# Kernel optimization log

Hardware: AMD Instinct MI355X
Metric: run time of the kernel (lower is better)

The kernel has to match this reference:

```python
import jax, jax.numpy as jnp
import numpy as np

FEATURES_NUM = 125388  # shogi halfKP: 81 king squares * 1548
L1, L2, L3 = 256, 32, 32
BATCH = 1024
ACTIVE = 38  # typical number of active halfKP features per position


def _sparse_multi_hot(key, batch, nfeat, active):
    idx = jax.random.randint(key, (batch, active), 0, nfeat)
    rows = jnp.arange(batch)[:, None]
    x = jnp.zeros((batch, nfeat), dtype=jnp.float32)
    return x.at[rows, idx].set(1.0)


def setup_inputs() -> dict:
    key = jax.random.key(0)
    ks = jax.random.split(key, 10)
    s_in = 1.0 / np.sqrt(FEATURES_NUM)
    s1 = 1.0 / np.sqrt(2 * L1)
    s2 = 1.0 / np.sqrt(L2)
    s3 = 1.0 / np.sqrt(L3)
    return {
        "x1": _sparse_multi_hot(ks[0], BATCH, FEATURES_NUM, ACTIVE),
        "x2": _sparse_multi_hot(ks[1], BATCH, FEATURES_NUM, ACTIVE),
        "W_in": jax.random.normal(ks[2], (FEATURES_NUM, L1), jnp.float32) * s_in,
        "b_in": jax.random.normal(ks[3], (L1,), jnp.float32) * s_in,
        "W1": jax.random.normal(ks[4], (2 * L1, L2), jnp.float32) * s1,
        "b1": jax.random.normal(ks[5], (L2,), jnp.float32) * s1,
        "W2": jax.random.normal(ks[6], (L2, L3), jnp.float32) * s2,
        "b2": jax.random.normal(ks[7], (L3,), jnp.float32) * s2,
        "Wo": jax.random.normal(ks[8], (L3, 1), jnp.float32) * s3,
        "bo": jax.random.normal(ks[9], (1,), jnp.float32) * s3,
    }


def reference(x1, x2, W_in, b_in, W1, b1, W2, b2, Wo, bo):
    # Feature transformer: shared input_layer on both perspectives.
    a1 = x1 @ W_in + b_in              # [B, L1]
    a2 = x2 @ W_in + b_in              # [B, L1]
    x = jnp.concatenate([a1, a2], axis=1)      # [B, 2*L1]
    x = jnp.clip(x, 0.0, 1.0)                   # clipped ReLU
    x = jnp.clip(x @ W1 + b1, 0.0, 1.0)         # [B, L2]
    x = jnp.clip(x @ W2 + b2, 0.0, 1.0)         # [B, L3]
    return x @ Wo + bo                          # [B, 1]
```

## Files before the change

### kernel.cpp

```cpp
#include <hip/hip_runtime.h>

#define FEAT  125388
#define VEC4  (FEAT / 4)
#define L1    256
#define L2    32
#define L3    32
#define BATCH 1024
#define CAP   64

typedef unsigned int uint4_ev __attribute__((ext_vector_type(4)));

__global__ __launch_bounds__(256) void nnue_scan_ft(
    const float* __restrict__ x1, const float* __restrict__ x2,
    const float* __restrict__ W_in, const float* __restrict__ b_in,
    float* __restrict__ x_cat)
{
    const int bp = blockIdx.x;
    const int b  = bp >> 1;
    const int p  = bp & 1;
    const int t  = threadIdx.x;

    __shared__ int s_idx[CAP];
    __shared__ int s_cnt;
    if (t == 0) s_cnt = 0;
    __syncthreads();

    const float* base = (p == 0 ? x1 : x2) + (size_t)b * FEAT;
    const uint4_ev* row = reinterpret_cast<const uint4_ev*>(base);

    for (int iv = t; iv < VEC4; iv += 256) {
        uint4_ev v = __builtin_nontemporal_load(&row[iv]);
        if (v.x | v.y | v.z | v.w) {
            #pragma unroll
            for (int c = 0; c < 4; ++c) {
                if (v[c] != 0u) {
                    int slot = atomicAdd(&s_cnt, 1);
                    if (slot < CAP) s_idx[slot] = iv * 4 + c;
                }
            }
        }
    }
    __syncthreads();

    const int n = min(s_cnt, CAP);
    float acc = b_in[t];
    for (int i = 0; i < n; ++i)
        acc += W_in[(size_t)s_idx[i] * L1 + t];

    x_cat[(size_t)b * (2 * L1) + p * L1 + t] = fminf(fmaxf(acc, 0.f), 1.f);
}

__global__ __launch_bounds__(256) void nnue_tail(
    const float* __restrict__ x_cat,
    const float* __restrict__ W1, const float* __restrict__ b1,
    const float* __restrict__ W2, const float* __restrict__ b2,
    const float* __restrict__ Wo, const float* __restrict__ bo,
    float* __restrict__ out)
{
    const int b = blockIdx.x;
    const int t = threadIdx.x;

    __shared__ float s_x[2 * L1];
    __shared__ float s_part[8][L2];
    __shared__ float s_y[L2];
    __shared__ float s_o[L3];

    s_x[t]       = x_cat[(size_t)b * (2 * L1) + t];
    s_x[t + 256] = x_cat[(size_t)b * (2 * L1) + 256 + t];
    __syncthreads();

    {
        const int j  = t & 31;
        const int p  = t >> 5;
        const int k0 = p * 64;
        float acc = 0.f;
        #pragma unroll 4
        for (int k = k0; k < k0 + 64; ++k)
            acc += s_x[k] * W1[k * L2 + j];
        s_part[p][j] = acc;
    }
    __syncthreads();
    if (t < L2) {
        float acc = b1[t];
        #pragma unroll
        for (int p = 0; p < 8; ++p) acc += s_part[p][t];
        s_y[t] = fminf(fmaxf(acc, 0.f), 1.f);
    }
    __syncthreads();
    if (t < L3) {
        float acc = b2[t];
        #pragma unroll
        for (int k = 0; k < L2; ++k) acc += s_y[k] * W2[k * L3 + t];
        s_o[t] = fminf(fmaxf(acc, 0.f), 1.f) * Wo[t];
    }
    __syncthreads();
    if (t == 0) {
        float acc = bo[0];
        #pragma unroll
        for (int k = 0; k < L3; ++k) acc += s_o[k];
        out[b] = acc;
    }
}

extern "C" void kernel_launch(void* const* d_in, const int* in_sizes, int n_in,
                              void* d_out, int out_size, void* d_ws, size_t ws_size,
                              hipStream_t stream) {
    const float* x1   = (const float*)d_in[0];
    const float* x2   = (const float*)d_in[1];
    const float* W_in = (const float*)d_in[2];
    const float* b_in = (const float*)d_in[3];
    const float* W1   = (const float*)d_in[4];
    const float* b1   = (const float*)d_in[5];
    const float* W2   = (const float*)d_in[6];
    const float* b2   = (const float*)d_in[7];
    const float* Wo   = (const float*)d_in[8];
    const float* bo   = (const float*)d_in[9];
    float* out   = (float*)d_out;
    float* x_cat = (float*)d_ws;

    nnue_scan_ft<<<2 * BATCH, 256, 0, stream>>>(x1, x2, W_in, b_in, x_cat);
    nnue_tail<<<BATCH, 256, 0, stream>>>(x_cat, W1, b1, W2, b2, Wo, bo, out);
}
```

Baseline: 179.8 us.

## Fuse scan/feature-transform and MLP tail via last-block atomic counter

Merges the two kernels into one. Each batch row's two perspective blocks increment a per-row atomic flag, and the second block to finish runs the small MLP tail using its own accumulator plus the partner's result from global memory. This removes the separate tail launch and one global reload, at the cost of a memset launch per call, threadfences, and extra shared memory per block.

Result: slower. 510.9 us (+184.2%).

```diff
diff --git a/kernel.cpp b/kernel.cpp
--- a/kernel.cpp
+++ b/kernel.cpp
@@ -10,24 +10,34 @@
 
 typedef unsigned int uint4_ev __attribute__((ext_vector_type(4)));
 
-__global__ __launch_bounds__(256) void nnue_scan_ft(
+__global__ __launch_bounds__(256) void nnue_fused(
     const float* __restrict__ x1, const float* __restrict__ x2,
     const float* __restrict__ W_in, const float* __restrict__ b_in,
-    float* __restrict__ x_cat)
+    const float* __restrict__ W1, const float* __restrict__ b1,
+    const float* __restrict__ W2, const float* __restrict__ b2,
+    const float* __restrict__ Wo, const float* __restrict__ bo,
+    float* __restrict__ x_cat,
+    int*   __restrict__ flags,
+    float* __restrict__ out)
 {
     const int bp = blockIdx.x;
     const int b  = bp >> 1;
     const int p  = bp & 1;
     const int t  = threadIdx.x;
 
-    __shared__ int s_idx[CAP];
-    __shared__ int s_cnt;
+    __shared__ int   s_idx[CAP];
+    __shared__ int   s_cnt;
+    __shared__ int   s_last;
+    __shared__ float s_x[2 * L1];
+    __shared__ float s_part[8][L2];
+    __shared__ float s_y[L2];
+    __shared__ float s_o[L3];
+
     if (t == 0) s_cnt = 0;
     __syncthreads();
 
     const float* base = (p == 0 ? x1 : x2) + (size_t)b * FEAT;
     const uint4_ev* row = reinterpret_cast<const uint4_ev*>(base);
-
     for (int iv = t; iv < VEC4; iv += 256) {
         uint4_ev v = __builtin_nontemporal_load(&row[iv]);
         if (v.x | v.y | v.z | v.w) {
@@ -46,59 +56,54 @@
     float acc = b_in[t];
     for (int i = 0; i < n; ++i)
         acc += W_in[(size_t)s_idx[i] * L1 + t];
+    const float v_own = fminf(fmaxf(acc, 0.f), 1.f);
 
-    x_cat[(size_t)b * (2 * L1) + p * L1 + t] = fminf(fmaxf(acc, 0.f), 1.f);
-}
+    x_cat[(size_t)b * (2 * L1) + p * L1 + t] = v_own;
+    __threadfence();
+    __syncthreads();
+    if (t == 0) {
+        int old = __hip_atomic_fetch_add(&flags[b], 1, __ATOMIC_ACQ_REL,
+                                         __HIP_MEMORY_SCOPE_AGENT);
+        s_last = old;
+    }
+    __syncthreads();
+    if (s_last != 1) return;
+    __threadfence();
 
-__global__ __launch_bounds__(256) void nnue_tail(
-    const float* __restrict__ x_cat,
-    const float* __restrict__ W1, const float* __restrict__ b1,
-    const float* __restrict__ W2, const float* __restrict__ b2,
-    const float* __restrict__ Wo, const float* __restrict__ bo,
-    float* __restrict__ out)
-{
-    const int b = blockIdx.x;
-    const int t = threadIdx.x;
-
-    __shared__ float s_x[2 * L1];
-    __shared__ float s_part[8][L2];
-    __shared__ float s_y[L2];
-    __shared__ float s_o[L3];
-
-    s_x[t]       = x_cat[(size_t)b * (2 * L1) + t];
-    s_x[t + 256] = x_cat[(size_t)b * (2 * L1) + 256 + t];
+    s_x[p * L1 + t]       = v_own;
+    s_x[(1 - p) * L1 + t] = x_cat[(size_t)b * (2 * L1) + (1 - p) * L1 + t];
     __syncthreads();
 
     {
         const int j  = t & 31;
-        const int p  = t >> 5;
-        const int k0 = p * 64;
-        float acc = 0.f;
+        const int pc = t >> 5;
+        const int k0 = pc * 64;
+        float a1 = 0.f;
         #pragma unroll 4
         for (int k = k0; k < k0 + 64; ++k)
-            acc += s_x[k] * W1[k * L2 + j];
-        s_part[p][j] = acc;
+            a1 += s_x[k] * W1[k * L2 + j];
+        s_part[pc][j] = a1;
     }
     __syncthreads();
     if (t < L2) {
-        float acc = b1[t];
+        float a1 = b1[t];
         #pragma unroll
-        for (int p = 0; p < 8; ++p) acc += s_part[p][t];
-        s_y[t] = fminf(fmaxf(acc, 0.f), 1.f);
+        for (int pc = 0; pc < 8; ++pc) a1 += s_part[pc][t];
+        s_y[t] = fminf(fmaxf(a1, 0.f), 1.f);
     }
     __syncthreads();
     if (t < L3) {
-        float acc = b2[t];
+        float a2 = b2[t];
         #pragma unroll
-        for (int k = 0; k < L2; ++k) acc += s_y[k] * W2[k * L3 + t];
-        s_o[t] = fminf(fmaxf(acc, 0.f), 1.f) * Wo[t];
+        for (int k = 0; k < L2; ++k) a2 += s_y[k] * W2[k * L3 + t];
+        s_o[t] = fminf(fmaxf(a2, 0.f), 1.f) * Wo[t];
     }
     __syncthreads();
     if (t == 0) {
-        float acc = bo[0];
+        float a3 = bo[0];
         #pragma unroll
-        for (int k = 0; k < L3; ++k) acc += s_o[k];
-        out[b] = acc;
+        for (int k = 0; k < L3; ++k) a3 += s_o[k];
+        out[b] = a3;
     }
 }
 
@@ -116,8 +121,11 @@
     const float* Wo   = (const float*)d_in[8];
     const float* bo   = (const float*)d_in[9];
     float* out   = (float*)d_out;
+
     float* x_cat = (float*)d_ws;
+    int*   flags = (int*)((char*)d_ws + (size_t)BATCH * 2 * L1 * sizeof(float));
 
-    nnue_scan_ft<<<2 * BATCH, 256, 0, stream>>>(x1, x2, W_in, b_in, x_cat);
-    nnue_tail<<<BATCH, 256, 0, stream>>>(x_cat, W1, b1, W2, b2, Wo, bo, out);
+    hipMemsetAsync(flags, 0, BATCH * sizeof(int), stream);
+    nnue_fused<<<2 * BATCH, 256, 0, stream>>>(
+        x1, x2, W_in, b_in, W1, b1, W2, b2, Wo, bo, x_cat, flags, out);
 }
```
